# Kernel optimization log

Measured on AMD Instinct MI355X. Metric: run time of the kernel, lower is better.

Reference implementation:

```python
import jax, jax.numpy as jnp
import numpy as np

B, N, H, L = 4, 200, 128, 3
HH = H // 2
VOC_E_IN, VOC_E_OUT, NODE_DIM = 3, 2, 2
EPS_BN = 1e-5


def masked_bn(x, m, gamma, beta):
    """BatchNorm1d (batch stats, no running stats) applied only to masked positions.
    x: (..., H), m: (...) float mask. Unmasked entries pass through unchanged."""
    mm = m[..., None]
    cnt = jnp.sum(m)
    axes = tuple(range(x.ndim - 1))
    mean = jnp.sum(x * mm, axis=axes) / cnt
    var = jnp.sum(((x - mean) ** 2) * mm, axis=axes) / cnt  # biased, as BatchNorm1d
    xn = (x - mean) * jax.lax.rsqrt(var + EPS_BN) * gamma + beta
    return jnp.where(mm > 0, xn, x)


def gcn_layer(x, e, mask, sq_mask, p, i):
    # EdgeFeatures: e_ij = U*e_ij + V*x_i + V*x_j (V*x masked)
    Ue = jnp.einsum('bijh,hk->bijk', e, p['eU_w'][i]) + p['eU_b'][i]
    Vx_e = mask[..., None] * (jnp.einsum('bnh,hk->bnk', x, p['eV_w'][i]) + p['eV_b'][i])
    e_tmp = Ue + Vx_e[:, :, None, :] + Vx_e[:, None, :, :]
    gate = jax.nn.sigmoid(e_tmp)
    # NodeFeatures (mean aggregation)
    Ux = mask[..., None] * (jnp.einsum('bnh,hk->bnk', x, p['nU_w'][i]) + p['nU_b'][i])
    Vx = mask[..., None] * (jnp.einsum('bnh,hk->bnk', x, p['nV_w'][i]) + p['nV_b'][i])
    gate_m = gate * sq_mask[..., None]
    agg = jnp.einsum('bijh,bjh->bih', gate_m, Vx)
    denom = jnp.sum(gate_m, axis=2)
    x_tmp = Ux + agg / (1e-20 + denom)
    # masked batchnorm + ReLU + residual
    e_bn = masked_bn(e_tmp, sq_mask, p['bnE_g'][i], p['bnE_b'][i])
    x_bn = masked_bn(x_tmp, mask, p['bnN_g'][i], p['bnN_b'][i])
    return x + jax.nn.relu(x_bn), e + jax.nn.relu(e_bn)


def forward(x_edges, x_edges_values, x_nodes_coord, mask, p):
    x = jnp.einsum('bnd,dh->bnh', x_nodes_coord, p['w_coord'])          # (B,N,H)
    e_val = x_edges_values[..., None] * p['w_eval'][0]                  # (B,N,N,HH)
    e_tag = p['emb_edge'][x_edges]                                      # (B,N,N,HH)
    e = jnp.concatenate([e_val, e_tag], axis=-1)                        # (B,N,N,H)
    sq_mask = mask[:, :, None] * mask[:, None, :]
    for i in range(L):
        x, e = gcn_layer(x, e, mask, sq_mask, p, i)
    # MLP on edges (mlp_layers=2 -> one hidden ReLU layer)
    h = jax.nn.relu(jnp.einsum('bijh,hk->bijk', e, p['mlp_U_w']) + p['mlp_U_b'])
    y = jnp.einsum('bijh,hk->bijk', h, p['mlp_V_w']) + p['mlp_V_b']     # (B,N,N,2)
    return y


def setup_inputs() -> dict:
    key = jax.random.key(0)
    ks = jax.random.split(key, 32)
    x_edges = jax.random.randint(ks[0], (B, N, N), 0, VOC_E_IN)
    x_edges_values = jax.random.uniform(ks[1], (B, N, N), dtype=jnp.float32)
    x_nodes_coord = jax.random.uniform(ks[2], (B, N, NODE_DIM), dtype=jnp.float32)
    # prefix mask: variable graph sizes padded to N (as ConvTSP builds)
    lens = jax.random.randint(ks[3], (B,), N // 2, N + 1)
    mask = (jnp.arange(N)[None, :] < lens[:, None]).astype(jnp.float32)
    s = 1.0 / np.sqrt(H)
    inp = dict(x_edges=x_edges, x_edges_values=x_edges_values,
               x_nodes_coord=x_nodes_coord, mask=mask,
               w_coord=jax.random.normal(ks[4], (NODE_DIM, H)) * 0.5,
               w_eval=jax.random.normal(ks[5], (1, HH)) * 0.5,
               emb_edge=jax.random.normal(ks[6], (VOC_E_IN, HH)) * 0.5,
               eU_w=jax.random.normal(ks[7], (L, H, H)) * s,
               eU_b=jnp.zeros((L, H)),
               eV_w=jax.random.normal(ks[8], (L, H, H)) * s,
               eV_b=jnp.zeros((L, H)),
               nU_w=jax.random.normal(ks[9], (L, H, H)) * s,
               nU_b=jnp.zeros((L, H)),
               nV_w=jax.random.normal(ks[10], (L, H, H)) * s,
               nV_b=jnp.zeros((L, H)),
               bnE_g=jnp.ones((L, H)), bnE_b=jnp.zeros((L, H)),
               bnN_g=jnp.ones((L, H)), bnN_b=jnp.zeros((L, H)),
               mlp_U_w=jax.random.normal(ks[11], (H, H)) * s,
               mlp_U_b=jnp.zeros((H,)),
               mlp_V_w=jax.random.normal(ks[12], (H, VOC_E_OUT)) * s,
               mlp_V_b=jnp.zeros((VOC_E_OUT,)))
    return inp


def reference(x_edges, x_edges_values, x_nodes_coord, mask,
              w_coord, w_eval, emb_edge,
              eU_w, eU_b, eV_w, eV_b, nU_w, nU_b, nV_w, nV_b,
              bnE_g, bnE_b, bnN_g, bnN_b,
              mlp_U_w, mlp_U_b, mlp_V_w, mlp_V_b):
    p = dict(w_coord=w_coord, w_eval=w_eval, emb_edge=emb_edge,
             eU_w=eU_w, eU_b=eU_b, eV_w=eV_w, eV_b=eV_b,
             nU_w=nU_w, nU_b=nU_b, nV_w=nV_w, nV_b=nV_b,
             bnE_g=bnE_g, bnE_b=bnE_b, bnN_g=bnN_g, bnN_b=bnN_b,
             mlp_U_w=mlp_U_w, mlp_U_b=mlp_U_b, mlp_V_w=mlp_V_w, mlp_V_b=mlp_V_b)
    return forward(x_edges, x_edges_values, x_nodes_coord, mask, p)
```

## Files before the change

kernel.cpp:

```cpp
#include <hip/hip_runtime.h>
#include <hip/hip_bf16.h>


typedef __hip_bfloat16 bf16;
typedef __attribute__((ext_vector_type(8))) short short8_t;
typedef __attribute__((ext_vector_type(4))) float f32x4;

#define B_ 4
#define N_ 200
#define H_ 128
#define BN_ (B_ * N_)
#define MT_ 13
#define MROWS_ 208

__device__ __forceinline__ unsigned short f2b(float f) {
  unsigned int i = __float_as_uint(f);
  i = (i + 0x7fffu + ((i >> 16) & 1u)) >> 16;
  return (unsigned short)i;
}
__device__ __forceinline__ float b2f16(unsigned short u) {
  return __uint_as_float((unsigned int)u << 16);
}


__global__ __launch_bounds__(128) void k_init_x(
    const float* __restrict__ coord, const float* __restrict__ w_coord,
    float* __restrict__ x) {
  int bi = blockIdx.x, h = threadIdx.x;
  float c0 = coord[bi * 2 + 0], c1 = coord[bi * 2 + 1];
  x[(size_t)bi * H_ + h] = c0 * w_coord[h] + c1 * w_coord[H_ + h];
}

__global__ __launch_bounds__(256) void k_cnt(const float* __restrict__ mask,
                                             float* __restrict__ cnts) {
  int t = threadIdx.x, b = t >> 6, l = t & 63;
  float s = 0.f;
  for (int n = l; n < N_; n += 64) s += mask[b * N_ + n];
#pragma unroll
  for (int d = 1; d < 64; d <<= 1) s += __shfl_xor(s, d);
  __shared__ float ms[B_];
  if (l == 0) ms[b] = s;
  __syncthreads();
  if (t == 0) {
    float cn = 0.f, ce = 0.f;
    for (int k = 0; k < B_; ++k) { cn += ms[k]; ce += ms[k] * ms[k]; }
    cnts[0] = cn; cnts[1] = ce;
  }
}

__global__ __launch_bounds__(256) void k_prep_w(const float* __restrict__ eUw,
                                                const float* __restrict__ mUw,
                                                bf16* __restrict__ WT) {
  int blk = blockIdx.x;
  const float* src = (blk < 3) ? (eUw + (size_t)blk * H_ * H_) : mUw;
  bf16* dst = WT + (size_t)blk * H_ * H_;
  for (int q = threadIdx.x; q < H_ * H_; q += 256) {
    int out = q >> 7, in = q & 127;
    dst[q] = __float2bfloat16(src[in * H_ + out]);
  }
}


__global__ __launch_bounds__(128) void k_node_lin(
    const float* __restrict__ x, const float* __restrict__ eVw,
    const float* __restrict__ eVb, const float* __restrict__ nUw,
    const float* __restrict__ nUb, const float* __restrict__ nVw,
    const float* __restrict__ nVb, const float* __restrict__ mask,
    float* __restrict__ Vxe, float* __restrict__ Ux, float* __restrict__ Vx) {
  __shared__ float xr[H_];
  int bi = blockIdx.x, h = threadIdx.x;
  xr[h] = x[(size_t)bi * H_ + h];
  __syncthreads();
  float m = mask[bi];
  float a = 0.f, bvv = 0.f, c = 0.f;
#pragma unroll 4
  for (int k = 0; k < H_; ++k) {
    float xv = xr[k];
    a   = fmaf(xv, eVw[k * H_ + h], a);
    bvv = fmaf(xv, nUw[k * H_ + h], bvv);
    c   = fmaf(xv, nVw[k * H_ + h], c);
  }
  Vxe[(size_t)bi * H_ + h] = m * (a + eVb[h]);
  Ux[(size_t)bi * H_ + h]  = m * (bvv + nUb[h]);
  Vx[(size_t)bi * H_ + h]  = m * (c + nVb[h]);
}


#define LDS_PUT(SA, ROW, K0, V)                                            \
  {                                                                        \
    unsigned int p0 = ((unsigned int)f2b((V).y) << 16) | f2b((V).x);       \
    unsigned int p1 = ((unsigned int)f2b((V).w) << 16) | f2b((V).z);       \
    unsigned long long pk = ((unsigned long long)p1 << 32) | p0;           \
    int byo = ((ROW) << 8) + ((((K0) * 2)) ^ (((ROW) & 7) << 4));          \
    *(unsigned long long*)((SA) + byo) = pk;                               \
  }


template <int MODE>
__global__ __launch_bounds__(256, 3) void k_edge(
    float* __restrict__ e, bf16* __restrict__ etmp,
    const float* __restrict__ ssPrev, const int* __restrict__ xe,
    const float* __restrict__ ev, const float* __restrict__ w_eval,
    const float* __restrict__ emb, const bf16* __restrict__ WT,
    const float* __restrict__ eUb, const float* __restrict__ Vxe,
    const float* __restrict__ Vx, const float* __restrict__ Ux,
    const float* __restrict__ mask, float* __restrict__ xtmp,
    float* __restrict__ sums) {
  __shared__ __align__(16) char sA[MROWS_ * 256];
  const int bi = blockIdx.x;
  const int b = bi / N_;
  const int t = threadIdx.x;
  const int lane = t & 63;
  const int w = t >> 6;
  const float mask_i = mask[bi];

  const int n0 = w << 5;
  const int colA = n0 + (lane & 15);
  const int colB = colA + 16;
  const int kgrp = (lane >> 4) << 3;
  short8_t bfA[4], bfB[4];
  {
    const short* w0 = (const short*)WT + colA * H_ + kgrp;
    const short* w1 = (const short*)WT + colB * H_ + kgrp;
#pragma unroll
    for (int kk = 0; kk < 4; ++kk) {
      bfA[kk] = *(const short8_t*)(w0 + kk * 32);
      bfB[kk] = *(const short8_t*)(w1 + kk * 32);
    }
  }

  {
    float* eb = e + (size_t)bi * N_ * H_;
    const unsigned short* tb =
        (const unsigned short*)etmp + (size_t)bi * N_ * H_;
    for (int q4 = t; q4 < MROWS_ * 32; q4 += 256) {
      int row = q4 >> 5, k0 = (q4 & 31) << 2;
      float4 v = make_float4(0.f, 0.f, 0.f, 0.f);
      if (row < N_) {
        if (MODE == 0) {
          if (k0 < 64) {
            float evv = ev[bi * N_ + row];
            v.x = evv * w_eval[k0 + 0];
            v.y = evv * w_eval[k0 + 1];
            v.z = evv * w_eval[k0 + 2];
            v.w = evv * w_eval[k0 + 3];
          } else {
            v = *(const float4*)(emb + xe[bi * N_ + row] * 64 + (k0 - 64));
          }
        } else {
          v = *(const float4*)(eb + row * H_ + k0);
          ushort4 tv = *(const ushort4*)(tb + row * H_ + k0);
          float mj = mask[b * N_ + row];
          bool msk = (mask_i * mj) > 0.f;
          float4 sc = *(const float4*)(ssPrev + k0);
          float4 sh = *(const float4*)(ssPrev + H_ + k0);
          float f0 = b2f16(tv.x), f1 = b2f16(tv.y);
          float f2 = b2f16(tv.z), f3 = b2f16(tv.w);
          v.x += fmaxf(msk ? fmaf(f0, sc.x, sh.x) : f0, 0.f);
          v.y += fmaxf(msk ? fmaf(f1, sc.y, sh.y) : f1, 0.f);
          v.z += fmaxf(msk ? fmaf(f2, sc.z, sh.z) : f2, 0.f);
          v.w += fmaxf(msk ? fmaf(f3, sc.w, sh.w) : f3, 0.f);
        }
        *(float4*)(eb + row * H_ + k0) = v;
      }
      LDS_PUT(sA, row, k0, v)
    }
  }
  __syncthreads();

  const float add0 = eUb[colA] + Vxe[(size_t)bi * H_ + colA];
  const float add1 = eUb[colB] + Vxe[(size_t)bi * H_ + colB];
  const float* VxeB = Vxe + (size_t)b * N_ * H_;
  const float* VxB  = Vx  + (size_t)b * N_ * H_;

  float agg0 = 0.f, agg1 = 0.f, den0 = 0.f, den1 = 0.f;
  float s1a = 0.f, s1b = 0.f, s2a = 0.f, s2b = 0.f;
  const int kb = (lane >> 4) << 4;

  for (int mt = 0; mt < MT_; ++mt) {
    f32x4 acc0 = {0.f, 0.f, 0.f, 0.f}, acc1 = {0.f, 0.f, 0.f, 0.f};
    int ra = mt * 16 + (lane & 15);
#pragma unroll
    for (int kk = 0; kk < 4; ++kk) {
      int ko = kk * 64 + kb;
      short8_t av = *(const short8_t*)(sA + (ra << 8) + (ko ^ ((ra & 7) << 4)));
      acc0 = __builtin_amdgcn_mfma_f32_16x16x32_bf16(av, bfA[kk], acc0, 0, 0, 0);
      acc1 = __builtin_amdgcn_mfma_f32_16x16x32_bf16(av, bfB[kk], acc1, 0, 0, 0);
    }
#pragma unroll
    for (int r = 0; r < 4; ++r) {
      int j = mt * 16 + ((lane >> 4) << 2) + r;
      bool valid = (j < N_);
      float mj = valid ? mask[b * N_ + j] : 0.f;
      float sqm = mask_i * mj;
      float vj0 = valid ? VxeB[(size_t)j * H_ + colA] : 0.f;
      float vj1 = valid ? VxeB[(size_t)j * H_ + colB] : 0.f;
      float t0 = acc0[r] + add0 + vj0;
      float t1 = acc1[r] + add1 + vj1;
      if (valid) {
        size_t o = ((size_t)bi * N_ + j) * H_;
        etmp[o + colA] = __float2bfloat16(t0);
        etmp[o + colB] = __float2bfloat16(t1);
      }
      float g0 = sqm / (1.f + __expf(-t0));
      float g1 = sqm / (1.f + __expf(-t1));
      float vx0 = valid ? VxB[(size_t)j * H_ + colA] : 0.f;
      float vx1 = valid ? VxB[(size_t)j * H_ + colB] : 0.f;
      agg0 = fmaf(g0, vx0, agg0);
      agg1 = fmaf(g1, vx1, agg1);
      den0 += g0; den1 += g1;
      s1a = fmaf(t0, sqm, s1a);
      s1b = fmaf(t1, sqm, s1b);
      s2a = fmaf(t0 * sqm, t0, s2a);
      s2b = fmaf(t1 * sqm, t1, s2b);
    }
  }
#pragma unroll
  for (int d = 16; d <= 32; d <<= 1) {
    agg0 += __shfl_xor(agg0, d); agg1 += __shfl_xor(agg1, d);
    den0 += __shfl_xor(den0, d); den1 += __shfl_xor(den1, d);
    s1a += __shfl_xor(s1a, d);   s1b += __shfl_xor(s1b, d);
    s2a += __shfl_xor(s2a, d);   s2b += __shfl_xor(s2b, d);
  }
  if ((lane >> 4) == 0) {
    atomicAdd(&sums[colA], s1a);
    atomicAdd(&sums[colB], s1b);
    atomicAdd(&sums[H_ + colA], s2a);
    atomicAdd(&sums[H_ + colB], s2b);
    float xt0 = Ux[(size_t)bi * H_ + colA] + agg0 / (1e-20f + den0);
    float xt1 = Ux[(size_t)bi * H_ + colB] + agg1 / (1e-20f + den1);
    xtmp[(size_t)bi * H_ + colA] = xt0;
    xtmp[(size_t)bi * H_ + colB] = xt1;
    atomicAdd(&sums[2 * H_ + colA], xt0 * mask_i);
    atomicAdd(&sums[3 * H_ + colA], xt0 * xt0 * mask_i);
    atomicAdd(&sums[2 * H_ + colB], xt1 * mask_i);
    atomicAdd(&sums[3 * H_ + colB], xt1 * xt1 * mask_i);
  }
}


__global__ __launch_bounds__(128) void k_stats(
    const float* __restrict__ sums, const float* __restrict__ cnts,
    const float* __restrict__ gE, const float* __restrict__ bE,
    const float* __restrict__ gN, const float* __restrict__ bN,
    float* __restrict__ ss) {
  int h = threadIdx.x;
  float cntN = cnts[0], cntE = cnts[1];
  float mE = sums[h] / cntE;
  float vE = sums[H_ + h] / cntE - mE * mE;
  float scE = gE[h] * rsqrtf(vE + 1e-5f);
  ss[h] = scE;
  ss[H_ + h] = bE[h] - mE * scE;
  float mN = sums[2 * H_ + h] / cntN;
  float vN = sums[3 * H_ + h] / cntN - mN * mN;
  float scN = gN[h] * rsqrtf(vN + 1e-5f);
  ss[2 * H_ + h] = scN;
  ss[3 * H_ + h] = bN[h] - mN * scN;
}

__global__ __launch_bounds__(128) void k_xupd(const float* __restrict__ xtmp,
                                              const float* __restrict__ mask,
                                              const float* __restrict__ ss,
                                              float* __restrict__ x) {
  int bi = blockIdx.x, h = threadIdx.x;
  float mi = mask[bi];
  float tv = xtmp[(size_t)bi * H_ + h];
  float xn = (mi > 0.f) ? fmaf(tv, ss[2 * H_ + h], ss[3 * H_ + h]) : tv;
  x[(size_t)bi * H_ + h] += fmaxf(xn, 0.f);
}


__global__ __launch_bounds__(256, 2) void k_head(
    const float* __restrict__ e, const bf16* __restrict__ etmp,
    const float* __restrict__ ssPrev, const bf16* __restrict__ UT,
    const float* __restrict__ Ub, const float* __restrict__ Vw,
    const float* __restrict__ Vb, const float* __restrict__ mask,
    float* __restrict__ y) {
  __shared__ __align__(16) char sA[MROWS_ * 256];
  __shared__ float part[4][MROWS_][2];
  const int bi = blockIdx.x;
  const int b = bi / N_;
  const int t = threadIdx.x;
  const int lane = t & 63;
  const int w = t >> 6;
  const float mask_i = mask[bi];

  const int n0 = w << 5;
  const int colA = n0 + (lane & 15);
  const int colB = colA + 16;
  const int kgrp = (lane >> 4) << 3;
  short8_t bfA[4], bfB[4];
  {
    const short* w0 = (const short*)UT + colA * H_ + kgrp;
    const short* w1 = (const short*)UT + colB * H_ + kgrp;
#pragma unroll
    for (int kk = 0; kk < 4; ++kk) {
      bfA[kk] = *(const short8_t*)(w0 + kk * 32);
      bfB[kk] = *(const short8_t*)(w1 + kk * 32);
    }
  }

  {
    const float* eb = e + (size_t)bi * N_ * H_;
    const unsigned short* tb =
        (const unsigned short*)etmp + (size_t)bi * N_ * H_;
    for (int q4 = t; q4 < MROWS_ * 32; q4 += 256) {
      int row = q4 >> 5, k0 = (q4 & 31) << 2;
      float4 v = make_float4(0.f, 0.f, 0.f, 0.f);
      if (row < N_) {
        v = *(const float4*)(eb + row * H_ + k0);
        ushort4 tv = *(const ushort4*)(tb + row * H_ + k0);
        float mj = mask[b * N_ + row];
        bool msk = (mask_i * mj) > 0.f;
        float4 sc = *(const float4*)(ssPrev + k0);
        float4 sh = *(const float4*)(ssPrev + H_ + k0);
        float f0 = b2f16(tv.x), f1 = b2f16(tv.y);
        float f2 = b2f16(tv.z), f3 = b2f16(tv.w);
        v.x += fmaxf(msk ? fmaf(f0, sc.x, sh.x) : f0, 0.f);
        v.y += fmaxf(msk ? fmaf(f1, sc.y, sh.y) : f1, 0.f);
        v.z += fmaxf(msk ? fmaf(f2, sc.z, sh.z) : f2, 0.f);
        v.w += fmaxf(msk ? fmaf(f3, sc.w, sh.w) : f3, 0.f);
      }
      LDS_PUT(sA, row, k0, v)
    }
  }
  __syncthreads();

  float bu0 = Ub[colA], bu1 = Ub[colB];
  float v00 = Vw[colA * 2], v01 = Vw[colA * 2 + 1];
  float v10 = Vw[colB * 2], v11 = Vw[colB * 2 + 1];
  const int kb = (lane >> 4) << 4;

  for (int mt = 0; mt < MT_; ++mt) {
    f32x4 acc0 = {0.f, 0.f, 0.f, 0.f}, acc1 = {0.f, 0.f, 0.f, 0.f};
    int ra = mt * 16 + (lane & 15);
#pragma unroll
    for (int kk = 0; kk < 4; ++kk) {
      int ko = kk * 64 + kb;
      short8_t av = *(const short8_t*)(sA + (ra << 8) + (ko ^ ((ra & 7) << 4)));
      acc0 = __builtin_amdgcn_mfma_f32_16x16x32_bf16(av, bfA[kk], acc0, 0, 0, 0);
      acc1 = __builtin_amdgcn_mfma_f32_16x16x32_bf16(av, bfB[kk], acc1, 0, 0, 0);
    }
#pragma unroll
    for (int r = 0; r < 4; ++r) {
      float h0v = fmaxf(acc0[r] + bu0, 0.f);
      float h1v = fmaxf(acc1[r] + bu1, 0.f);
      float p0 = h0v * v00 + h1v * v10;
      float p1 = h0v * v01 + h1v * v11;
#pragma unroll
      for (int d = 1; d < 16; d <<= 1) {
        p0 += __shfl_xor(p0, d);
        p1 += __shfl_xor(p1, d);
      }
      int j = mt * 16 + ((lane >> 4) << 2) + r;
      if ((lane & 15) == 0) { part[w][j][0] = p0; part[w][j][1] = p1; }
    }
  }
  __syncthreads();
  float vb0 = Vb[0], vb1 = Vb[1];
  for (int q = t; q < N_ * 2; q += 256) {
    int j = q >> 1, c = q & 1;
    float s = part[0][j][c] + part[1][j][c] + part[2][j][c] + part[3][j][c] +
              (c ? vb1 : vb0);
    y[((size_t)bi * N_ + j) * 2 + c] = s;
  }
}


extern "C" void kernel_launch(void* const* d_in, const int* in_sizes, int n_in,
                              void* d_out, int out_size, void* d_ws,
                              size_t ws_size, hipStream_t stream) {
  const int*   x_edges = (const int*)d_in[0];
  const float* ev      = (const float*)d_in[1];
  const float* coord   = (const float*)d_in[2];
  const float* mask    = (const float*)d_in[3];
  const float* w_coord = (const float*)d_in[4];
  const float* w_eval  = (const float*)d_in[5];
  const float* emb     = (const float*)d_in[6];
  const float* eUw = (const float*)d_in[7];
  const float* eUb = (const float*)d_in[8];
  const float* eVw = (const float*)d_in[9];
  const float* eVb = (const float*)d_in[10];
  const float* nUw = (const float*)d_in[11];
  const float* nUb = (const float*)d_in[12];
  const float* nVw = (const float*)d_in[13];
  const float* nVb = (const float*)d_in[14];
  const float* gE  = (const float*)d_in[15];
  const float* bE  = (const float*)d_in[16];
  const float* gN  = (const float*)d_in[17];
  const float* bN  = (const float*)d_in[18];
  const float* mUw = (const float*)d_in[19];
  const float* mUb = (const float*)d_in[20];
  const float* mVw = (const float*)d_in[21];
  const float* mVb = (const float*)d_in[22];

  char* ws = (char*)d_ws;
  size_t off = 0;
  auto alloc = [&](size_t bytes) {
    void* p = ws + off;
    off += (bytes + 255) & ~(size_t)255;
    return p;
  };
  float* e    = (float*)alloc((size_t)B_ * N_ * N_ * H_ * 4);
  bf16* etmp  = (bf16*)alloc((size_t)B_ * N_ * N_ * H_ * 2);
  float* x    = (float*)alloc((size_t)BN_ * H_ * 4);
  float* Vxe  = (float*)alloc((size_t)BN_ * H_ * 4);
  float* Ux   = (float*)alloc((size_t)BN_ * H_ * 4);
  float* Vx   = (float*)alloc((size_t)BN_ * H_ * 4);
  float* xtmp = (float*)alloc((size_t)BN_ * H_ * 4);
  float* sums = (float*)alloc(4 * H_ * 4);
  float* ss   = (float*)alloc(4 * H_ * 4);
  float* cnts = (float*)alloc(256);
  bf16* WT    = (bf16*)alloc((size_t)4 * H_ * H_ * 2);

  k_prep_w<<<4, 256, 0, stream>>>(eUw, mUw, WT);
  k_init_x<<<BN_, 128, 0, stream>>>(coord, w_coord, x);
  k_cnt<<<1, 256, 0, stream>>>(mask, cnts);

  for (int l = 0; l < 3; ++l) {
    size_t wo = (size_t)l * H_ * H_;
    size_t bo = (size_t)l * H_;
    hipMemsetAsync(sums, 0, 4 * H_ * 4, stream);
    k_node_lin<<<BN_, 128, 0, stream>>>(x, eVw + wo, eVb + bo, nUw + wo,
                                        nUb + bo, nVw + wo, nVb + bo, mask,
                                        Vxe, Ux, Vx);
    if (l == 0) {
      k_edge<0><<<BN_, 256, 0, stream>>>(e, etmp, ss, x_edges, ev, w_eval,
                                         emb, WT + wo, eUb + bo, Vxe, Vx, Ux,
                                         mask, xtmp, sums);
    } else {
      k_edge<1><<<BN_, 256, 0, stream>>>(e, etmp, ss, x_edges, ev, w_eval,
                                         emb, WT + wo, eUb + bo, Vxe, Vx, Ux,
                                         mask, xtmp, sums);
    }
    k_stats<<<1, 128, 0, stream>>>(sums, cnts, gE + bo, bE + bo, gN + bo,
                                   bN + bo, ss);
    if (l < 2) k_xupd<<<BN_, 128, 0, stream>>>(xtmp, mask, ss, x);
  }
  k_head<<<BN_, 256, 0, stream>>>(e, etmp, ss, WT + (size_t)3 * H_ * H_, mUb,
                                  mVw, mVb, mask, (float*)d_out);
}
```

Baseline: 405.3 us.

## Split edge and head kernels across four j-tiles per row with atomic aggregation

Each (b,i) row of the edge and head kernels is now split into four blocks covering row tiles of 64 or 48 j-rows. This shrinks LDS per block from 52KB to 16KB, raises the occupancy hint, and quadruples the grid. Partial agg/den sums are combined with global atomics into buffers zeroed by the node-linear kernel, and a new k_xfin kernel computes x_tmp and the node BN sums. This costs extra atomics and one more launch per layer. It also skips x_tmp in the last layer, where it was unused.

```diff
diff --git a/kernel.cpp b/kernel.cpp
--- a/kernel.cpp
+++ b/kernel.cpp
@@ -10,8 +10,8 @@
 #define N_ 200
 #define H_ 128
 #define BN_ (B_ * N_)
-#define MT_ 13
-#define MROWS_ 208
+#define JT_ 4
+#define MAXROWS_ 64
 
 __device__ __forceinline__ unsigned short f2b(float f) {
   unsigned int i = __float_as_uint(f);
@@ -66,10 +66,13 @@
     const float* __restrict__ eVb, const float* __restrict__ nUw,
     const float* __restrict__ nUb, const float* __restrict__ nVw,
     const float* __restrict__ nVb, const float* __restrict__ mask,
-    float* __restrict__ Vxe, float* __restrict__ Ux, float* __restrict__ Vx) {
+    float* __restrict__ Vxe, float* __restrict__ Ux, float* __restrict__ Vx,
+    float* __restrict__ agg, float* __restrict__ den) {
   __shared__ float xr[H_];
   int bi = blockIdx.x, h = threadIdx.x;
   xr[h] = x[(size_t)bi * H_ + h];
+  agg[(size_t)bi * H_ + h] = 0.f;
+  den[(size_t)bi * H_ + h] = 0.f;
   __syncthreads();
   float m = mask[bi];
   float a = 0.f, bvv = 0.f, c = 0.f;
@@ -85,37 +88,38 @@
   Vx[(size_t)bi * H_ + h]  = m * (c + nVb[h]);
 }
 
-
-#define LDS_PUT(SA, ROW, K0, V)                                            \
+#define LDS_PUT(SA, LR, K0, V)                                             \
   {                                                                        \
     unsigned int p0 = ((unsigned int)f2b((V).y) << 16) | f2b((V).x);       \
     unsigned int p1 = ((unsigned int)f2b((V).w) << 16) | f2b((V).z);       \
     unsigned long long pk = ((unsigned long long)p1 << 32) | p0;           \
-    int byo = ((ROW) << 8) + ((((K0) * 2)) ^ (((ROW) & 7) << 4));          \
+    int byo = ((LR) << 8) + ((((K0) * 2)) ^ (((LR) & 7) << 4));            \
     *(unsigned long long*)((SA) + byo) = pk;                               \
   }
 
 
 template <int MODE>
-__global__ __launch_bounds__(256, 3) void k_edge(
+__global__ __launch_bounds__(256, 6) void k_edge(
     float* __restrict__ e, bf16* __restrict__ etmp,
     const float* __restrict__ ssPrev, const int* __restrict__ xe,
     const float* __restrict__ ev, const float* __restrict__ w_eval,
     const float* __restrict__ emb, const bf16* __restrict__ WT,
     const float* __restrict__ eUb, const float* __restrict__ Vxe,
-    const float* __restrict__ Vx, const float* __restrict__ Ux,
-    const float* __restrict__ mask, float* __restrict__ xtmp,
+    const float* __restrict__ Vx, const float* __restrict__ mask,
+    float* __restrict__ agg, float* __restrict__ den,
     float* __restrict__ sums) {
-  __shared__ __align__(16) char sA[MROWS_ * 256];
-  const int bi = blockIdx.x;
+  __shared__ __align__(16) char sA[MAXROWS_ * 256];
+  const int bi = blockIdx.x >> 2;
+  const int jh = blockIdx.x & 3;
+  const int mt0 = (jh == 0) ? 0 : 3 * jh + 1;
+  const int mt1 = 3 * jh + 4;
   const int b = bi / N_;
   const int t = threadIdx.x;
   const int lane = t & 63;
   const int w = t >> 6;
   const float mask_i = mask[bi];
 
-  const int n0 = w << 5;
-  const int colA = n0 + (lane & 15);
+  const int colA = (w << 5) + (lane & 15);
   const int colB = colA + 16;
   const int kgrp = (lane >> 4) << 3;
   short8_t bfA[4], bfB[4];
@@ -130,11 +134,13 @@
   }
 
   {
+    const int nrt = (mt1 - mt0) << 4;
     float* eb = e + (size_t)bi * N_ * H_;
     const unsigned short* tb =
         (const unsigned short*)etmp + (size_t)bi * N_ * H_;
-    for (int q4 = t; q4 < MROWS_ * 32; q4 += 256) {
-      int row = q4 >> 5, k0 = (q4 & 31) << 2;
+    for (int q4 = t; q4 < nrt * 32; q4 += 256) {
+      int lr = q4 >> 5, k0 = (q4 & 31) << 2;
+      int row = (mt0 << 4) + lr;
       float4 v = make_float4(0.f, 0.f, 0.f, 0.f);
       if (row < N_) {
         if (MODE == 0) {
@@ -163,7 +169,7 @@
         }
         *(float4*)(eb + row * H_ + k0) = v;
       }
-      LDS_PUT(sA, row, k0, v)
+      LDS_PUT(sA, lr, k0, v)
     }
   }
   __syncthreads();
@@ -177,9 +183,9 @@
   float s1a = 0.f, s1b = 0.f, s2a = 0.f, s2b = 0.f;
   const int kb = (lane >> 4) << 4;
 
-  for (int mt = 0; mt < MT_; ++mt) {
+  for (int mt = mt0; mt < mt1; ++mt) {
     f32x4 acc0 = {0.f, 0.f, 0.f, 0.f}, acc1 = {0.f, 0.f, 0.f, 0.f};
-    int ra = mt * 16 + (lane & 15);
+    int ra = ((mt - mt0) << 4) + (lane & 15);
 #pragma unroll
     for (int kk = 0; kk < 4; ++kk) {
       int ko = kk * 64 + kb;
@@ -189,7 +195,7 @@
     }
 #pragma unroll
     for (int r = 0; r < 4; ++r) {
-      int j = mt * 16 + ((lane >> 4) << 2) + r;
+      int j = (mt << 4) + ((lane >> 4) << 2) + r;
       bool valid = (j < N_);
       float mj = valid ? mask[b * N_ + j] : 0.f;
       float sqm = mask_i * mj;
@@ -227,15 +233,25 @@
     atomicAdd(&sums[colB], s1b);
     atomicAdd(&sums[H_ + colA], s2a);
     atomicAdd(&sums[H_ + colB], s2b);
-    float xt0 = Ux[(size_t)bi * H_ + colA] + agg0 / (1e-20f + den0);
-    float xt1 = Ux[(size_t)bi * H_ + colB] + agg1 / (1e-20f + den1);
-    xtmp[(size_t)bi * H_ + colA] = xt0;
-    xtmp[(size_t)bi * H_ + colB] = xt1;
-    atomicAdd(&sums[2 * H_ + colA], xt0 * mask_i);
-    atomicAdd(&sums[3 * H_ + colA], xt0 * xt0 * mask_i);
-    atomicAdd(&sums[2 * H_ + colB], xt1 * mask_i);
-    atomicAdd(&sums[3 * H_ + colB], xt1 * xt1 * mask_i);
-  }
+    atomicAdd(&agg[(size_t)bi * H_ + colA], agg0);
+    atomicAdd(&agg[(size_t)bi * H_ + colB], agg1);
+    atomicAdd(&den[(size_t)bi * H_ + colA], den0);
+    atomicAdd(&den[(size_t)bi * H_ + colB], den1);
+  }
+}
+
+
+__global__ __launch_bounds__(128) void k_xfin(
+    const float* __restrict__ agg, const float* __restrict__ den,
+    const float* __restrict__ Ux, const float* __restrict__ mask,
+    float* __restrict__ xtmp, float* __restrict__ sums) {
+  int bi = blockIdx.x, h = threadIdx.x;
+  float mi = mask[bi];
+  float xt = Ux[(size_t)bi * H_ + h] +
+             agg[(size_t)bi * H_ + h] / (1e-20f + den[(size_t)bi * H_ + h]);
+  xtmp[(size_t)bi * H_ + h] = xt;
+  atomicAdd(&sums[2 * H_ + h], xt * mi);
+  atomicAdd(&sums[3 * H_ + h], xt * xt * mi);
 }
 
 
@@ -270,23 +286,25 @@
 }
 
 
-__global__ __launch_bounds__(256, 2) void k_head(
+__global__ __launch_bounds__(256, 6) void k_head(
     const float* __restrict__ e, const bf16* __restrict__ etmp,
     const float* __restrict__ ssPrev, const bf16* __restrict__ UT,
     const float* __restrict__ Ub, const float* __restrict__ Vw,
     const float* __restrict__ Vb, const float* __restrict__ mask,
     float* __restrict__ y) {
-  __shared__ __align__(16) char sA[MROWS_ * 256];
-  __shared__ float part[4][MROWS_][2];
-  const int bi = blockIdx.x;
+  __shared__ __align__(16) char sA[MAXROWS_ * 256];
+  __shared__ float part[4][MAXROWS_][2];
+  const int bi = blockIdx.x >> 2;
+  const int jh = blockIdx.x & 3;
+  const int mt0 = (jh == 0) ? 0 : 3 * jh + 1;
+  const int mt1 = 3 * jh + 4;
   const int b = bi / N_;
   const int t = threadIdx.x;
   const int lane = t & 63;
   const int w = t >> 6;
   const float mask_i = mask[bi];
 
-  const int n0 = w << 5;
-  const int colA = n0 + (lane & 15);
+  const int colA = (w << 5) + (lane & 15);
   const int colB = colA + 16;
   const int kgrp = (lane >> 4) << 3;
   short8_t bfA[4], bfB[4];
@@ -301,11 +319,13 @@
   }
 
   {
+    const int nrt = (mt1 - mt0) << 4;
     const float* eb = e + (size_t)bi * N_ * H_;
     const unsigned short* tb =
         (const unsigned short*)etmp + (size_t)bi * N_ * H_;
-    for (int q4 = t; q4 < MROWS_ * 32; q4 += 256) {
-      int row = q4 >> 5, k0 = (q4 & 31) << 2;
+    for (int q4 = t; q4 < nrt * 32; q4 += 256) {
+      int lr = q4 >> 5, k0 = (q4 & 31) << 2;
+      int row = (mt0 << 4) + lr;
       float4 v = make_float4(0.f, 0.f, 0.f, 0.f);
       if (row < N_) {
         v = *(const float4*)(eb + row * H_ + k0);
@@ -321,7 +341,7 @@
         v.z += fmaxf(msk ? fmaf(f2, sc.z, sh.z) : f2, 0.f);
         v.w += fmaxf(msk ? fmaf(f3, sc.w, sh.w) : f3, 0.f);
       }
-      LDS_PUT(sA, row, k0, v)
+      LDS_PUT(sA, lr, k0, v)
     }
   }
   __syncthreads();
@@ -331,9 +351,9 @@
   float v10 = Vw[colB * 2], v11 = Vw[colB * 2 + 1];
   const int kb = (lane >> 4) << 4;
 
-  for (int mt = 0; mt < MT_; ++mt) {
+  for (int mt = mt0; mt < mt1; ++mt) {
     f32x4 acc0 = {0.f, 0.f, 0.f, 0.f}, acc1 = {0.f, 0.f, 0.f, 0.f};
-    int ra = mt * 16 + (lane & 15);
+    int ra = ((mt - mt0) << 4) + (lane & 15);
 #pragma unroll
     for (int kk = 0; kk < 4; ++kk) {
       int ko = kk * 64 + kb;
@@ -352,17 +372,21 @@
         p0 += __shfl_xor(p0, d);
         p1 += __shfl_xor(p1, d);
       }
-      int j = mt * 16 + ((lane >> 4) << 2) + r;
-      if ((lane & 15) == 0) { part[w][j][0] = p0; part[w][j][1] = p1; }
+      int jl = ((mt - mt0) << 4) + ((lane >> 4) << 2) + r;
+      if ((lane & 15) == 0) { part[w][jl][0] = p0; part[w][jl][1] = p1; }
     }
   }
   __syncthreads();
   float vb0 = Vb[0], vb1 = Vb[1];
-  for (int q = t; q < N_ * 2; q += 256) {
-    int j = q >> 1, c = q & 1;
-    float s = part[0][j][c] + part[1][j][c] + part[2][j][c] + part[3][j][c] +
-              (c ? vb1 : vb0);
-    y[((size_t)bi * N_ + j) * 2 + c] = s;
+  const int nrt = (mt1 - mt0) << 4;
+  for (int q = t; q < nrt * 2; q += 256) {
+    int jl = q >> 1, c = q & 1;
+    int j = (mt0 << 4) + jl;
+    if (j < N_) {
+      float s = part[0][jl][c] + part[1][jl][c] + part[2][jl][c] +
+                part[3][jl][c] + (c ? vb1 : vb0);
+      y[((size_t)bi * N_ + j) * 2 + c] = s;
+    }
   }
 }
 
@@ -408,6 +432,8 @@
   float* Ux   = (float*)alloc((size_t)BN_ * H_ * 4);
   float* Vx   = (float*)alloc((size_t)BN_ * H_ * 4);
   float* xtmp = (float*)alloc((size_t)BN_ * H_ * 4);
+  float* agg  = (float*)alloc((size_t)BN_ * H_ * 4);
+  float* den  = (float*)alloc((size_t)BN_ * H_ * 4);
   float* sums = (float*)alloc(4 * H_ * 4);
   float* ss   = (float*)alloc(4 * H_ * 4);
   float* cnts = (float*)alloc(256);
@@ -423,20 +449,23 @@
     hipMemsetAsync(sums, 0, 4 * H_ * 4, stream);
     k_node_lin<<<BN_, 128, 0, stream>>>(x, eVw + wo, eVb + bo, nUw + wo,
                                         nUb + bo, nVw + wo, nVb + bo, mask,
-                                        Vxe, Ux, Vx);
+                                        Vxe, Ux, Vx, agg, den);
     if (l == 0) {
-      k_edge<0><<<BN_, 256, 0, stream>>>(e, etmp, ss, x_edges, ev, w_eval,
-                                         emb, WT + wo, eUb + bo, Vxe, Vx, Ux,
-                                         mask, xtmp, sums);
+      k_edge<0><<<BN_ * JT_, 256, 0, stream>>>(
+          e, etmp, ss, x_edges, ev, w_eval, emb, WT + wo, eUb + bo, Vxe, Vx,
+          mask, agg, den, sums);
     } else {
-      k_edge<1><<<BN_, 256, 0, stream>>>(e, etmp, ss, x_edges, ev, w_eval,
-                                         emb, WT + wo, eUb + bo, Vxe, Vx, Ux,
-                                         mask, xtmp, sums);
-    }
+      k_edge<1><<<BN_ * JT_, 256, 0, stream>>>(
+          e, etmp, ss, x_edges, ev, w_eval, emb, WT + wo, eUb + bo, Vxe, Vx,
+          mask, agg, den, sums);
+    }
+    if (l < 2)
+      k_xfin<<<BN_, 128, 0, stream>>>(agg, den, Ux, mask, xtmp, sums);
     k_stats<<<1, 128, 0, stream>>>(sums, cnts, gE + bo, bE + bo, gN + bo,
                                    bN + bo, ss);
     if (l < 2) k_xupd<<<BN_, 128, 0, stream>>>(xtmp, mask, ss, x);
   }
-  k_head<<<BN_, 256, 0, stream>>>(e, etmp, ss, WT + (size_t)3 * H_ * H_, mUb,
-                                  mVw, mVb, mask, (float*)d_out);
-}
+  k_head<<<BN_ * JT_, 256, 0, stream>>>(e, etmp, ss,
+                                        WT + (size_t)3 * H_ * H_, mUb, mVw,
+                                        mVb, mask, (float*)d_out);
+}
```

After: 515.9 us. +27.3%, slower.
